# Performance work log

Hardware: AMD Instinct MI355X
Metric: run time of the kernel (lower is better)

## Reference

```python
import jax, jax.numpy as jnp
import numpy as np

# HGIN_classifier: two relational-GIN layers with ReLU between.
# FastRGIN layer math (relational GIN, eps=0, single-linear MLP):
#   agg_r[i] = sum_{(j->i) with edge_type r} x[j]          (per-relation neighbor sum)
#   out[i]   = (1+eps) * x[i] @ W_self + sum_r agg_r[i] @ W_r + b

N = 100000      # nodes
E = 1600000     # edges (avg degree 16)
R = 2           # relations (follower / following)
DIN, DH, DOUT = 128, 256, 2
EPS = 0.0


def setup_inputs() -> dict:
    key = jax.random.key(0)
    ks = jax.random.split(key, 8)
    x = jax.random.normal(ks[0], (N, DIN), dtype=jnp.float32)
    edge_index = jax.random.randint(ks[1], (2, E), 0, N, dtype=jnp.int64)
    edge_type = jax.random.randint(ks[2], (E,), 0, R, dtype=jnp.int64)
    s1 = 1.0 / np.sqrt(DIN).astype(np.float32)
    s2 = 1.0 / np.sqrt(DH).astype(np.float32)
    w1_self = jax.random.normal(ks[3], (DIN, DH), jnp.float32) * s1
    w1_rel = jax.random.normal(ks[4], (R, DIN, DH), jnp.float32) * s1
    b1 = jnp.zeros((DH,), jnp.float32)
    w2_self = jax.random.normal(ks[5], (DH, DOUT), jnp.float32) * s2
    w2_rel = jax.random.normal(ks[6], (R, DH, DOUT), jnp.float32) * s2
    b2 = jnp.zeros((DOUT,), jnp.float32)
    return {"x": x, "edge_index": edge_index, "edge_type": edge_type,
            "w1_self": w1_self, "w1_rel": w1_rel, "b1": b1,
            "w2_self": w2_self, "w2_rel": w2_rel, "b2": b2}


def _rgin_layer(x, src, dst, etype, w_self, w_rel, b):
    n = x.shape[0]
    r = w_rel.shape[0]
    # fused (node, relation) segment id so one segment_sum handles all relations
    seg = dst * r + etype                                   # [E]
    agg = jax.ops.segment_sum(x[src], seg, num_segments=n * r)  # [N*R, d_in]
    agg = agg.reshape(n, r, -1)                              # [N, R, d_in]
    return (1.0 + EPS) * (x @ w_self) + jnp.einsum('nri,rio->no', agg, w_rel) + b


def reference(x, edge_index, edge_type, w1_self, w1_rel, b1, w2_self, w2_rel, b2):
    src, dst = edge_index[0], edge_index[1]
    h = jax.nn.relu(_rgin_layer(x, src, dst, edge_type, w1_self, w1_rel, b1))
    out = _rgin_layer(h, src, dst, edge_type, w2_self, w2_rel, b2)
    return out
```

## Files before the change

kernel.cpp:

```cpp
#include <hip/hip_runtime.h>


typedef _Float16 f16;
typedef _Float16 f16x2 __attribute__((ext_vector_type(2)));
typedef _Float16 f16x4 __attribute__((ext_vector_type(4)));
typedef _Float16 f16x8 __attribute__((ext_vector_type(8)));
typedef float    f32x4 __attribute__((ext_vector_type(4)));

constexpr int NN   = 100000;
constexpr int NR   = NN * 2;
constexpr int NB   = 512;
constexpr int BSH  = 9;
constexpr int CHUNK = 8192;

__global__ void zero_small(int* __restrict__ gcnt) {
  int t = threadIdx.x;
  if (t < NB) gcnt[t] = 0;
}

__global__ void bucketA(const int* __restrict__ dst, const int* __restrict__ et,
                        int* __restrict__ gcnt, int E) {
  __shared__ int h[NB];
  int t = threadIdx.x;
  for (int b = t; b < NB; b += 256) h[b] = 0;
  __syncthreads();
  int lo = blockIdx.x * CHUNK, hi = min(E, lo + CHUNK);
  for (int e = lo + t; e < hi; e += 256)
    atomicAdd(&h[(dst[e] * 2 + et[e]) >> BSH], 1);
  __syncthreads();
  for (int b = t; b < NB; b += 256) {
    int c = h[b];
    if (c) atomicAdd(&gcnt[b], c);
  }
}

__global__ void bscan(const int* __restrict__ gcnt, int* __restrict__ bstart,
                      int* __restrict__ gbase) {
  __shared__ int s[NB];
  int t = threadIdx.x;
  int v = gcnt[t];
  s[t] = v;
  __syncthreads();
  #pragma unroll
  for (int o = 1; o < NB; o <<= 1) {
    int u = (t >= o) ? s[t - o] : 0;
    __syncthreads();
    s[t] += u;
    __syncthreads();
  }
  bstart[t] = s[t] - v;
  gbase[t]  = s[t] - v;
  if (t == NB - 1) bstart[NB] = s[t];
}

__global__ void bucketB(const int* __restrict__ src, const int* __restrict__ dst,
                        const int* __restrict__ et, int* __restrict__ gbase,
                        int2* __restrict__ ebuf, int E) {
  __shared__ int h[NB], base[NB];
  int t = threadIdx.x;
  for (int b = t; b < NB; b += 256) h[b] = 0;
  __syncthreads();
  int lo = blockIdx.x * CHUNK, hi = min(E, lo + CHUNK);
  for (int e = lo + t; e < hi; e += 256)
    atomicAdd(&h[(dst[e] * 2 + et[e]) >> BSH], 1);
  __syncthreads();
  for (int b = t; b < NB; b += 256) {
    int c = h[b];
    base[b] = c ? atomicAdd(&gbase[b], c) : 0;
    h[b] = 0;
  }
  __syncthreads();
  for (int e = lo + t; e < hi; e += 256) {
    int seg = dst[e] * 2 + et[e];
    int b = seg >> BSH;
    int r = atomicAdd(&h[b], 1);
    ebuf[base[b] + r] = make_int2(src[e], seg);
  }
}

__global__ void bucketC(const int2* __restrict__ ebuf, const int* __restrict__ bstart,
                        int* __restrict__ off, int* __restrict__ srcs) {
  __shared__ int sh[NB], soff[NB], cnt[NB], tmp[256];
  int b = blockIdx.x, t = threadIdx.x;
  int lo = bstart[b], hi = bstart[b + 1];
  for (int s0 = t; s0 < NB; s0 += 256) { sh[s0] = 0; cnt[s0] = 0; }
  __syncthreads();
  for (int e = lo + t; e < hi; e += 256)
    atomicAdd(&sh[ebuf[e].y - (b << BSH)], 1);
  __syncthreads();
  int a0 = sh[2 * t], a1 = sh[2 * t + 1];
  tmp[t] = a0 + a1;
  __syncthreads();
  #pragma unroll
  for (int o = 1; o < 256; o <<= 1) {
    int u = (t >= o) ? tmp[t - o] : 0;
    __syncthreads();
    tmp[t] += u;
    __syncthreads();
  }
  int ex = tmp[t] - (a0 + a1);
  soff[2 * t] = ex;
  soff[2 * t + 1] = ex + a0;
  __syncthreads();
  int g0 = (b << BSH) + 2 * t;
  if (g0 <= NR)     off[g0]     = lo + soff[2 * t];
  if (g0 + 1 <= NR) off[g0 + 1] = lo + soff[2 * t + 1];
  for (int e = lo + t; e < hi; e += 256) {
    int2 p = ebuf[e];
    int s = p.y - (b << BSH);
    int r = atomicAdd(&cnt[s], 1);
    srcs[lo + soff[s] + r] = p.x;
  }
}

__global__ void cvt_x(const float4* __restrict__ xf, f16* __restrict__ xh, int n4) {
  int i = blockIdx.x * blockDim.x + threadIdx.x;
  if (i >= n4) return;
  float4 v = xf[i];
  f16x4 h;
  h.x = (f16)v.x; h.y = (f16)v.y; h.z = (f16)v.z; h.w = (f16)v.w;
  *(f16x4*)(xh + (size_t)i * 4) = h;
}

__global__ void cvt_w(const float* __restrict__ w1s, const float* __restrict__ w1r,
                      f16* __restrict__ w1t) {
  int id = blockIdx.x * blockDim.x + threadIdx.x;
  if (id >= 12 * 256 * 32) return;
  int ks = id >> 13, rem = id & 8191;
  int n = rem >> 5, ki = rem & 31;
  int k = ks * 32 + ki;
  float v = (k < 128) ? w1s[k * 256 + n] : w1r[(k - 128) * 256 + n];
  w1t[id] = (f16)v;
}

__global__ void aggregate(const f16* __restrict__ xh, const int* __restrict__ off,
                          const int* __restrict__ srcs, f16* __restrict__ aggh) {
  int w = (blockIdx.x * blockDim.x + threadIdx.x) >> 6;
  if (w >= NN) return;
  int lane = threadIdx.x & 63;
  int e0 = off[2 * w];
  int e1 = off[2 * w + 1];
  int e2 = off[2 * w + 2];
  float a0 = 0.f, a1 = 0.f, c0 = 0.f, c1 = 0.f;
  int e = e0;
  for (; e + 3 < e1; e += 4) {
    f16x2 v0 = *(const f16x2*)(xh + (long)srcs[e] * 128 + lane * 2);
    f16x2 v1 = *(const f16x2*)(xh + (long)srcs[e + 1] * 128 + lane * 2);
    f16x2 v2 = *(const f16x2*)(xh + (long)srcs[e + 2] * 128 + lane * 2);
    f16x2 v3 = *(const f16x2*)(xh + (long)srcs[e + 3] * 128 + lane * 2);
    a0 += (float)v0.x + (float)v1.x + (float)v2.x + (float)v3.x;
    a1 += (float)v0.y + (float)v1.y + (float)v2.y + (float)v3.y;
  }
  for (; e < e1; ++e) {
    f16x2 v = *(const f16x2*)(xh + (long)srcs[e] * 128 + lane * 2);
    a0 += (float)v.x; a1 += (float)v.y;
  }
  e = e1;
  for (; e + 3 < e2; e += 4) {
    f16x2 v0 = *(const f16x2*)(xh + (long)srcs[e] * 128 + lane * 2);
    f16x2 v1 = *(const f16x2*)(xh + (long)srcs[e + 1] * 128 + lane * 2);
    f16x2 v2 = *(const f16x2*)(xh + (long)srcs[e + 2] * 128 + lane * 2);
    f16x2 v3 = *(const f16x2*)(xh + (long)srcs[e + 3] * 128 + lane * 2);
    c0 += (float)v0.x + (float)v1.x + (float)v2.x + (float)v3.x;
    c1 += (float)v0.y + (float)v1.y + (float)v2.y + (float)v3.y;
  }
  for (; e < e2; ++e) {
    f16x2 v = *(const f16x2*)(xh + (long)srcs[e] * 128 + lane * 2);
    c0 += (float)v.x; c1 += (float)v.y;
  }
  f16* row = aggh + (long)w * 256;
  f16x2 o0; o0.x = (f16)a0; o0.y = (f16)a1;
  f16x2 o1; o1.x = (f16)c0; o1.y = (f16)c1;
  *(f16x2*)(row + lane * 2) = o0;
  *(f16x2*)(row + 128 + lane * 2) = o1;
}

__global__ __launch_bounds__(256, 2) void gemm_mfma(
    const f16* __restrict__ xh, const f16* __restrict__ aggh,
    const f16* __restrict__ w1t,
    const float* __restrict__ b1, const float* __restrict__ w2s,
    const float* __restrict__ w2r, const float* __restrict__ b2,
    float* __restrict__ z2, float* __restrict__ out) {
  __shared__ __align__(16) f16 Ash[2][128 * 40];
  __shared__ __align__(16) f16 Bsh[2][256 * 40];
  __shared__ float zbuf[2][128][6];
  const int t = threadIdx.x;
  const long rowBase = (long)blockIdx.x * 128;
  const int lane = t & 63, wv = t >> 6;
  const int rg = wv >> 1, cg = wv & 1;
  const int ml = lane & 15, quad = lane >> 4;

  f32x4 acc[4][8];
  #pragma unroll
  for (int mt = 0; mt < 4; ++mt)
    #pragma unroll
    for (int nt = 0; nt < 8; ++nt) acc[mt][nt] = (f32x4)(0.f);

  uint4 av[2], bv[4];
  auto load_tile = [&](int ks) {
    const int kt = ks * 32;
    #pragma unroll
    for (int c = 0; c < 2; ++c) {
      int g = c * 256 + t;
      int r = g >> 2, ch = g & 3;
      long grow = rowBase + r;
      if (grow < NN) {
        int k0 = kt + ch * 8;
        const f16* ap = (kt < 128) ? (xh + grow * 128 + k0)
                                   : (aggh + grow * 256 + (k0 - 128));
        av[c] = *(const uint4*)ap;
      } else {
        av[c] = make_uint4(0, 0, 0, 0);
      }
    }
    const uint4* bp = (const uint4*)(w1t + (long)ks * 8192) + t;
    #pragma unroll
    for (int c = 0; c < 4; ++c) bv[c] = bp[c * 256];
  };
  auto store_tile = [&](int buf) {
    #pragma unroll
    for (int c = 0; c < 2; ++c) {
      int g = c * 256 + t;
      int r = g >> 2, ch = g & 3;
      *(uint4*)&Ash[buf][r * 40 + ch * 8] = av[c];
    }
    #pragma unroll
    for (int c = 0; c < 4; ++c) {
      int g = c * 256 + t;
      int n = g >> 2, ch = g & 3;
      *(uint4*)&Bsh[buf][n * 40 + ch * 8] = bv[c];
    }
  };

  load_tile(0);
  store_tile(0);
  __syncthreads();

  for (int ks = 0; ks < 12; ++ks) {
    const int cur = ks & 1;
    if (ks < 11) load_tile(ks + 1);

    f16x8 af[4], bf[8];
    #pragma unroll
    for (int mt = 0; mt < 4; ++mt)
      af[mt] = *(const f16x8*)&Ash[cur][(rg * 64 + mt * 16 + ml) * 40 + quad * 8];
    #pragma unroll
    for (int nt = 0; nt < 8; ++nt)
      bf[nt] = *(const f16x8*)&Bsh[cur][(cg * 128 + nt * 16 + ml) * 40 + quad * 8];
    #pragma unroll
    for (int mt = 0; mt < 4; ++mt)
      #pragma unroll
      for (int nt = 0; nt < 8; ++nt)
        acc[mt][nt] = __builtin_amdgcn_mfma_f32_16x16x32_f16(af[mt], bf[nt],
                                                             acc[mt][nt], 0, 0, 0);
    if (ks < 11) store_tile(1 - cur);
    __syncthreads();
  }

  #pragma unroll
  for (int mt = 0; mt < 4; ++mt) {
    float z[4][6];
    #pragma unroll
    for (int rr = 0; rr < 4; ++rr)
      #pragma unroll
      for (int p = 0; p < 6; ++p) z[rr][p] = 0.f;
    #pragma unroll
    for (int nt = 0; nt < 8; ++nt) {
      int col = cg * 128 + nt * 16 + ml;
      float bb = b1[col];
      float wA = w2r[col * 2 + 0];
      float wB = w2r[col * 2 + 1];
      float wC = w2r[512 + col * 2 + 0];
      float wD = w2r[512 + col * 2 + 1];
      float wE = w2s[col * 2 + 0];
      float wF = w2s[col * 2 + 1];
      #pragma unroll
      for (int rr = 0; rr < 4; ++rr) {
        float h = acc[mt][nt][rr] + bb;
        h = h > 0.f ? h : 0.f;
        z[rr][0] = fmaf(h, wA, z[rr][0]);
        z[rr][1] = fmaf(h, wB, z[rr][1]);
        z[rr][2] = fmaf(h, wC, z[rr][2]);
        z[rr][3] = fmaf(h, wD, z[rr][3]);
        z[rr][4] = fmaf(h, wE, z[rr][4]);
        z[rr][5] = fmaf(h, wF, z[rr][5]);
      }
    }
    #pragma unroll
    for (int rr = 0; rr < 4; ++rr)
      #pragma unroll
      for (int p = 0; p < 6; ++p) {
        float v = z[rr][p];
        v += __shfl_xor(v, 1);
        v += __shfl_xor(v, 2);
        v += __shfl_xor(v, 4);
        v += __shfl_xor(v, 8);
        if (ml == 0) zbuf[cg][rg * 64 + mt * 16 + quad * 4 + rr][p] = v;
      }
  }
  __syncthreads();
  for (int i = t; i < 768; i += 256) {
    int r = i / 6, p = i % 6;
    long grow = rowBase + r;
    if (grow < NN) {
      float v = zbuf[0][r][p] + zbuf[1][r][p];
      if (p < 4) z2[grow * 4 + p] = v;
      else       out[grow * 2 + (p - 4)] = v + b2[p - 4];
    }
  }
}

__global__ void gather2(const float* __restrict__ z2, const int* __restrict__ off,
                        const int* __restrict__ srcs, float* __restrict__ out) {
  int tid = blockIdx.x * blockDim.x + threadIdx.x;
  int n = tid >> 2;
  if (n >= NN) return;
  int sub = tid & 3;
  int e0 = off[2 * n];
  int e1 = off[2 * n + 1];
  int e2 = off[2 * n + 2];
  float o0 = 0.f, o1 = 0.f;
  for (int e = e0 + sub; e < e1; e += 4) {
    float2 v = *(const float2*)(z2 + (long)srcs[e] * 4);
    o0 += v.x; o1 += v.y;
  }
  for (int e = e1 + sub; e < e2; e += 4) {
    float2 v = *(const float2*)(z2 + (long)srcs[e] * 4 + 2);
    o0 += v.x; o1 += v.y;
  }
  o0 += __shfl_xor(o0, 1); o1 += __shfl_xor(o1, 1);
  o0 += __shfl_xor(o0, 2); o1 += __shfl_xor(o1, 2);
  if (sub == 0) {
    out[n * 2 + 0] += o0;
    out[n * 2 + 1] += o1;
  }
}

extern "C" void kernel_launch(void* const* d_in, const int* in_sizes, int n_in,
                              void* d_out, int out_size, void* d_ws, size_t ws_size,
                              hipStream_t stream) {
  const float* x   = (const float*)d_in[0];
  const int*   ei  = (const int*)d_in[1];
  const int*   et  = (const int*)d_in[2];
  const float* w1s = (const float*)d_in[3];
  const float* w1r = (const float*)d_in[4];
  const float* b1  = (const float*)d_in[5];
  const float* w2s = (const float*)d_in[6];
  const float* w2r = (const float*)d_in[7];
  const float* b2  = (const float*)d_in[8];
  float* out = (float*)d_out;
  const int E = in_sizes[2];
  const int* src = ei;
  const int* dst = ei + E;

  f16*   aggh = (f16*)d_ws;
  f16*   xh   = aggh + (size_t)NN * 256;
  f16*   w1t  = xh + (size_t)NN * 128;
  float* z2   = (float*)(w1t + 12 * 256 * 32);
  int2*  ebuf = (int2*)(z2 + (size_t)NN * 4);
  int*   srcs = (int*)(ebuf + E);
  int*   off  = srcs + E;
  int*   gcnt = off + NR + 1;
  int*   bstart = gcnt + NB;
  int*   gbase  = bstart + NB + 1;

  int nblk = (E + CHUNK - 1) / CHUNK;
  zero_small<<<1, 512, 0, stream>>>(gcnt);
  bucketA<<<nblk, 256, 0, stream>>>(dst, et, gcnt, E);
  bscan<<<1, 512, 0, stream>>>(gcnt, bstart, gbase);
  bucketB<<<nblk, 256, 0, stream>>>(src, dst, et, gbase, ebuf, E);
  bucketC<<<NB, 256, 0, stream>>>(ebuf, bstart, off, srcs);

  int n4 = NN * 128 / 4;
  cvt_x<<<(n4 + 255) / 256, 256, 0, stream>>>((const float4*)x, xh, n4);
  cvt_w<<<(12 * 256 * 32 + 255) / 256, 256, 0, stream>>>(w1s, w1r, w1t);

  aggregate<<<(NN * 64 + 255) / 256, 256, 0, stream>>>(xh, off, srcs, aggh);

  gemm_mfma<<<(NN + 127) / 128, 256, 0, stream>>>(xh, aggh, w1t, b1, w2s, w2r, b2,
                                                  z2, out);

  gather2<<<(NN * 4 + 255) / 256, 256, 0, stream>>>(z2, off, srcs, out);
}
```

Measured before the change: 372.3 us.

## Drop LDS staging in layer-1 GEMM; load MFMA fragments directly from global

The fused GEMM no longer double-buffers A and B tiles through shared memory with a barrier every k-step. Each wave now owns a 64-column slice over 64 rows per block and reads its MFMA fragments straight from global memory (or L2), with the k-loop fully unrolled and no syncs. The block tile shrinks from 128 to 64 rows, so twice as many blocks launch, and the second-layer projection partials are reduced across four waves instead of two. The cost is that all four waves re-read the same A rows and there are more uncoalesced 16-byte global loads, traded against removing the LDS traffic and barrier stalls.

```diff
diff --git a/kernel.cpp b/kernel.cpp
--- a/kernel.cpp
+++ b/kernel.cpp
@@ -175,86 +175,51 @@
   *(f16x2*)(row + 128 + lane * 2) = o1;
 }
 
-__global__ __launch_bounds__(256, 2) void gemm_mfma(
+__global__ __launch_bounds__(256) void gemm_mfma(
     const f16* __restrict__ xh, const f16* __restrict__ aggh,
     const f16* __restrict__ w1t,
     const float* __restrict__ b1, const float* __restrict__ w2s,
     const float* __restrict__ w2r, const float* __restrict__ b2,
     float* __restrict__ z2, float* __restrict__ out) {
-  __shared__ __align__(16) f16 Ash[2][128 * 40];
-  __shared__ __align__(16) f16 Bsh[2][256 * 40];
-  __shared__ float zbuf[2][128][6];
+  __shared__ float zbuf[4][64][6];
   const int t = threadIdx.x;
-  const long rowBase = (long)blockIdx.x * 128;
   const int lane = t & 63, wv = t >> 6;
-  const int rg = wv >> 1, cg = wv & 1;
   const int ml = lane & 15, quad = lane >> 4;
-
-  f32x4 acc[4][8];
+  const long rowBase = (long)blockIdx.x * 64;
+
+  long rowc[4];
+  #pragma unroll
+  for (int mt = 0; mt < 4; ++mt) {
+    long r = rowBase + mt * 16 + ml;
+    rowc[mt] = r < NN ? r : (NN - 1);
+  }
+  const f16* bbase = w1t + (long)(wv * 64 + ml) * 32 + quad * 8;
+
+  f32x4 acc[4][4];
   #pragma unroll
   for (int mt = 0; mt < 4; ++mt)
     #pragma unroll
-    for (int nt = 0; nt < 8; ++nt) acc[mt][nt] = (f32x4)(0.f);
-
-  uint4 av[2], bv[4];
-  auto load_tile = [&](int ks) {
-    const int kt = ks * 32;
-    #pragma unroll
-    for (int c = 0; c < 2; ++c) {
-      int g = c * 256 + t;
-      int r = g >> 2, ch = g & 3;
-      long grow = rowBase + r;
-      if (grow < NN) {
-        int k0 = kt + ch * 8;
-        const f16* ap = (kt < 128) ? (xh + grow * 128 + k0)
-                                   : (aggh + grow * 256 + (k0 - 128));
-        av[c] = *(const uint4*)ap;
-      } else {
-        av[c] = make_uint4(0, 0, 0, 0);
-      }
+    for (int nt = 0; nt < 4; ++nt) acc[mt][nt] = (f32x4)(0.f);
+
+  #pragma unroll
+  for (int ks = 0; ks < 12; ++ks) {
+    f16x8 af[4], bf[4];
+    #pragma unroll
+    for (int mt = 0; mt < 4; ++mt) {
+      const f16* ap = (ks < 4)
+          ? (xh + rowc[mt] * 128 + ks * 32 + quad * 8)
+          : (aggh + rowc[mt] * 256 + (ks - 4) * 32 + quad * 8);
+      af[mt] = *(const f16x8*)ap;
     }
-    const uint4* bp = (const uint4*)(w1t + (long)ks * 8192) + t;
-    #pragma unroll
-    for (int c = 0; c < 4; ++c) bv[c] = bp[c * 256];
-  };
-  auto store_tile = [&](int buf) {
-    #pragma unroll
-    for (int c = 0; c < 2; ++c) {
-      int g = c * 256 + t;
-      int r = g >> 2, ch = g & 3;
-      *(uint4*)&Ash[buf][r * 40 + ch * 8] = av[c];
-    }
-    #pragma unroll
-    for (int c = 0; c < 4; ++c) {
-      int g = c * 256 + t;
-      int n = g >> 2, ch = g & 3;
-      *(uint4*)&Bsh[buf][n * 40 + ch * 8] = bv[c];
-    }
-  };
-
-  load_tile(0);
-  store_tile(0);
-  __syncthreads();
-
-  for (int ks = 0; ks < 12; ++ks) {
-    const int cur = ks & 1;
-    if (ks < 11) load_tile(ks + 1);
-
-    f16x8 af[4], bf[8];
-    #pragma unroll
-    for (int mt = 0; mt < 4; ++mt)
-      af[mt] = *(const f16x8*)&Ash[cur][(rg * 64 + mt * 16 + ml) * 40 + quad * 8];
-    #pragma unroll
-    for (int nt = 0; nt < 8; ++nt)
-      bf[nt] = *(const f16x8*)&Bsh[cur][(cg * 128 + nt * 16 + ml) * 40 + quad * 8];
+    #pragma unroll
+    for (int nt = 0; nt < 4; ++nt)
+      bf[nt] = *(const f16x8*)(bbase + (long)ks * 8192 + nt * 16 * 32);
     #pragma unroll
     for (int mt = 0; mt < 4; ++mt)
       #pragma unroll
-      for (int nt = 0; nt < 8; ++nt)
+      for (int nt = 0; nt < 4; ++nt)
         acc[mt][nt] = __builtin_amdgcn_mfma_f32_16x16x32_f16(af[mt], bf[nt],
                                                              acc[mt][nt], 0, 0, 0);
-    if (ks < 11) store_tile(1 - cur);
-    __syncthreads();
   }
 
   #pragma unroll
@@ -265,8 +230,8 @@
       #pragma unroll
       for (int p = 0; p < 6; ++p) z[rr][p] = 0.f;
     #pragma unroll
-    for (int nt = 0; nt < 8; ++nt) {
-      int col = cg * 128 + nt * 16 + ml;
+    for (int nt = 0; nt < 4; ++nt) {
+      int col = wv * 64 + nt * 16 + ml;
       float bb = b1[col];
       float wA = w2r[col * 2 + 0];
       float wB = w2r[col * 2 + 1];
@@ -295,15 +260,15 @@
         v += __shfl_xor(v, 2);
         v += __shfl_xor(v, 4);
         v += __shfl_xor(v, 8);
-        if (ml == 0) zbuf[cg][rg * 64 + mt * 16 + quad * 4 + rr][p] = v;
+        if (ml == 0) zbuf[wv][mt * 16 + quad * 4 + rr][p] = v;
       }
   }
   __syncthreads();
-  for (int i = t; i < 768; i += 256) {
+  for (int i = t; i < 384; i += 256) {
     int r = i / 6, p = i % 6;
     long grow = rowBase + r;
     if (grow < NN) {
-      float v = zbuf[0][r][p] + zbuf[1][r][p];
+      float v = zbuf[0][r][p] + zbuf[1][r][p] + zbuf[2][r][p] + zbuf[3][r][p];
       if (p < 4) z2[grow * 4 + p] = v;
       else       out[grow * 2 + (p - 4)] = v + b2[p - 4];
     }
@@ -377,8 +342,8 @@
 
   aggregate<<<(NN * 64 + 255) / 256, 256, 0, stream>>>(xh, off, srcs, aggh);
 
-  gemm_mfma<<<(NN + 127) / 128, 256, 0, stream>>>(xh, aggh, w1t, b1, w2s, w2r, b2,
-                                                  z2, out);
+  gemm_mfma<<<(NN + 63) / 64, 256, 0, stream>>>(xh, aggh, w1t, b1, w2s, w2r, b2,
+                                                z2, out);
 
   gather2<<<(NN * 4 + 255) / 256, 256, 0, stream>>>(z2, off, srcs, out);
 }
```

After: 385.9 us. 1.04x slower.
